# Kernel tuning notes

Hardware: AMD Instinct MI355X
Metric: run time of the kernel (lower is better)

## Reference

```python
import jax, jax.numpy as jnp
import numpy as np

D_MODEL = 1024
N_HEADS = 16
FEATURE_DIM = 16
HEAD_DIM = D_MODEL // N_HEADS  # 64
EPS = 1e-12


def taylor_exp(x):
    """2nd-order Taylor feature map of exp(q^T k / sqrt(d)).
    x: (b, h, l, d) -> (b, h, l, 1 + d + d^2)"""
    d = x.shape[-1]
    rd = jnp.sqrt(jnp.asarray(d, x.dtype))      # sqrt(d)
    rrd = jnp.sqrt(rd)                          # d^(1/4)
    r2 = jnp.sqrt(jnp.asarray(2.0, x.dtype))
    x2 = (x[..., :, None] * x[..., None, :]).reshape(*x.shape[:-1], d * d) / r2
    ones = jnp.ones_like(x[..., :1])
    return jnp.concatenate([ones, x / rrd, x2 / rd], axis=-1)


def setup_inputs() -> dict:
    key = jax.random.key(0)
    k0, k1, k2, k3, k4 = jax.random.split(key, 5)
    b, l = 1, 1024
    scale = 1.0 / np.sqrt(D_MODEL)
    hidden_states = jax.random.normal(k0, (b, l, D_MODEL), dtype=jnp.float32)
    Wq = jax.random.normal(k1, (N_HEADS * FEATURE_DIM, D_MODEL), dtype=jnp.float32) * scale
    Wk = jax.random.normal(k2, (N_HEADS * FEATURE_DIM, D_MODEL), dtype=jnp.float32) * scale
    Wv = jax.random.normal(k3, (N_HEADS * HEAD_DIM, D_MODEL), dtype=jnp.float32) * scale
    Wo = jax.random.normal(k4, (D_MODEL, N_HEADS * HEAD_DIM), dtype=jnp.float32) * scale
    return {"hidden_states": hidden_states, "Wq": Wq, "Wk": Wk, "Wv": Wv, "Wo": Wo}


def reference(hidden_states, Wq, Wk, Wv, Wo):
    b, l, _ = hidden_states.shape
    # projections (bias-free)
    q = (hidden_states @ Wq.T).reshape(b, l, N_HEADS, FEATURE_DIM).transpose(0, 2, 1, 3)
    k = (hidden_states @ Wk.T).reshape(b, l, N_HEADS, FEATURE_DIM).transpose(0, 2, 1, 3)
    v = (hidden_states @ Wv.T).reshape(b, l, N_HEADS, HEAD_DIM).transpose(0, 2, 1, 3)
    qf = taylor_exp(q)   # (b, h, l, D) with D = 1 + d + d^2 = 273
    kf = taylor_exp(k)
    # causal linear attention via associative KV accumulation
    # kv_state[l] = sum_{t<=l} phi(k_t) outer v_t  -> (b, h, l, head_dim, D)
    kv_state = jnp.cumsum(kf[..., None, :] * v[..., :, None], axis=2)
    num = jnp.einsum('bhlD,bhldD->bhld', qf, kv_state)
    den = jnp.einsum('bhlD,bhlD->bhl', qf, jnp.cumsum(kf, axis=2))[..., None] + EPS
    y = num / den                                # (b, h, l, head_dim)
    y = y.transpose(0, 2, 1, 3).reshape(b, l, N_HEADS * HEAD_DIM)
    return y @ Wo.T
```

## Files before the change

kernel.cpp:

```cpp
#include <hip/hip_runtime.h>

#define LSEQ 1024
#define DMODEL 1024
#define NHEADS 16
#define FDIM 16
#define HDIM 64
#define CHUNK 64
#define NCHUNK 16

typedef __attribute__((ext_vector_type(8))) short short8;
typedef __attribute__((ext_vector_type(4))) float floatx4;

__device__ __forceinline__ float bf2f(unsigned short u) {
    unsigned int x = ((unsigned int)u) << 16;
    return __builtin_bit_cast(float, x);
}
__device__ __forceinline__ unsigned short f2bf(float f) {
    unsigned int x = __builtin_bit_cast(unsigned int, f);
    unsigned int r = (x + 0x7fffu + ((x >> 16) & 1u)) >> 16;
    return (unsigned short)r;
}

__device__ __forceinline__ int block_detect_fp32(const unsigned short* wq) {
    __shared__ int cnt;
    if (threadIdx.x == 0) cnt = 0;
    __syncthreads();
    int bad = 0;
    for (int i = threadIdx.x; i < 1024; i += blockDim.x) {
        int e = (wq[i] >> 7) & 0xFF;
        if (e >= 143 || (e > 0 && e <= 80)) bad++;
    }
    if (bad) atomicAdd(&cnt, bad);
    __syncthreads();
    return cnt > 128;
}

#define U_QB   0
#define U_KB   262144
#define U_VB   524288
#define U_YB   1572864

#define MFMA(a, b, c) __builtin_amdgcn_mfma_f32_16x16x32_bf16((a), (b), (c), 0, 0, 0)

__device__ __forceinline__ void gemm64_body(
    unsigned short (&As)[64][136], unsigned short (&Bs)[64][136],
    const void* Araw, int a_fp32, int arow0,
    const void* Braw, int b_fp32, int brow0, floatx4 acc[4]) {
    int t = threadIdx.x;
    int r = t >> 2, c0 = (t & 3) * 32;
    int wave = t >> 6, lane = t & 63;
    int ml = lane & 15, q4 = lane >> 4;
    int mq = (wave >> 1) * 32, nq = (wave & 1) * 32;
    #pragma unroll
    for (int i = 0; i < 4; ++i) acc[i] = (floatx4){0.f, 0.f, 0.f, 0.f};

    short8 av[2][4], bv[2][4];
    auto stage = [&](int k0, short8 a[4], short8 b[4]) {
        if (!a_fp32) {
            const unsigned short* Ap = (const unsigned short*)Araw + (size_t)(arow0 + r) * DMODEL + k0 + c0;
            #pragma unroll
            for (int j = 0; j < 4; ++j) a[j] = *(const short8*)(Ap + j * 8);
        } else {
            const float* Ap = (const float*)Araw + (size_t)(arow0 + r) * DMODEL + k0 + c0;
            #pragma unroll
            for (int j = 0; j < 4; ++j)
                #pragma unroll
                for (int u = 0; u < 8; ++u) a[j][u] = (short)f2bf(Ap[j * 8 + u]);
        }
        if (!b_fp32) {
            const unsigned short* Bp = (const unsigned short*)Braw + (size_t)(brow0 + r) * DMODEL + k0 + c0;
            #pragma unroll
            for (int j = 0; j < 4; ++j) b[j] = *(const short8*)(Bp + j * 8);
        } else {
            const float* Bp = (const float*)Braw + (size_t)(brow0 + r) * DMODEL + k0 + c0;
            #pragma unroll
            for (int j = 0; j < 4; ++j)
                #pragma unroll
                for (int u = 0; u < 8; ++u) b[j][u] = (short)f2bf(Bp[j * 8 + u]);
        }
    };

    stage(0, av[0], bv[0]);
    stage(128, av[1], bv[1]);
    #pragma unroll
    for (int it = 0; it < 8; ++it) {
        int pp = it & 1;
        __syncthreads();
        #pragma unroll
        for (int j = 0; j < 4; ++j) {
            *(short8*)&As[r][c0 + j * 8] = av[pp][j];
            *(short8*)&Bs[r][c0 + j * 8] = bv[pp][j];
        }
        __syncthreads();
        if (it < 6) stage((it + 2) * 128, av[pp], bv[pp]);
        #pragma unroll
        for (int kk = 0; kk < 4; ++kk) {
            short8 a0 = *(const short8*)&As[mq + ml][kk * 32 + q4 * 8];
            short8 a1 = *(const short8*)&As[mq + 16 + ml][kk * 32 + q4 * 8];
            short8 b0 = *(const short8*)&Bs[nq + ml][kk * 32 + q4 * 8];
            short8 b1 = *(const short8*)&Bs[nq + 16 + ml][kk * 32 + q4 * 8];
            acc[0] = MFMA(a0, b0, acc[0]); acc[1] = MFMA(a0, b1, acc[1]);
            acc[2] = MFMA(a1, b0, acc[2]); acc[3] = MFMA(a1, b1, acc[3]);
        }
    }
}

__global__ __launch_bounds__(256) void qkv_gemm(
    const void* __restrict__ hidR, const void* __restrict__ WqR,
    const void* __restrict__ WkR, const void* __restrict__ WvR,
    unsigned short* __restrict__ qb, unsigned short* __restrict__ kb,
    unsigned short* __restrict__ vb) {
    int fp32 = block_detect_fp32((const unsigned short*)WqR);
    __shared__ __align__(16) unsigned short As[64][136];
    __shared__ __align__(16) unsigned short Bs[64][136];
    int nb = blockIdx.x, mb = blockIdx.y;
    const void* Braw; unsigned short* Cout; int ldc, col0, br0;
    if (nb < 4)      { Braw = WqR; br0 = nb * 64;       Cout = qb; ldc = 256;  col0 = nb * 64; }
    else if (nb < 8) { Braw = WkR; br0 = (nb - 4) * 64; Cout = kb; ldc = 256;  col0 = (nb - 4) * 64; }
    else             { Braw = WvR; br0 = (nb - 8) * 64; Cout = vb; ldc = 1024; col0 = (nb - 8) * 64; }

    floatx4 acc[4];
    gemm64_body(As, Bs, hidR, fp32, mb * 64, Braw, fp32, br0, acc);

    int wave = threadIdx.x >> 6, lane = threadIdx.x & 63;
    int ml = lane & 15, q4 = lane >> 4;
    int mq = (wave >> 1) * 32, nq = (wave & 1) * 32;
    #pragma unroll
    for (int mi = 0; mi < 2; ++mi)
        #pragma unroll
        for (int ni = 0; ni < 2; ++ni) {
            floatx4 a = acc[mi * 2 + ni];
            int nloc = nq + ni * 16 + ml;
            #pragma unroll
            for (int r4 = 0; r4 < 4; ++r4) {
                int row = mb * 64 + mq + mi * 16 + q4 * 4 + r4;
                Cout[(size_t)row * ldc + col0 + nloc] = f2bf(a[r4]);
            }
        }
}

__global__ __launch_bounds__(256) void flash_attn(
    const unsigned short* __restrict__ qb, const unsigned short* __restrict__ kb,
    const unsigned short* __restrict__ vb, unsigned short* __restrict__ ybB) {
    int h = blockIdx.x & 15, c = blockIdx.x >> 4;
    int l0 = c * CHUNK;
    __shared__ __align__(16) unsigned short qs[64][40];
    __shared__ __align__(16) unsigned short ksm[64][40];
    __shared__ __align__(16) unsigned short vT[80][72];
    __shared__ __align__(16) unsigned short P[64][72];
    int t = threadIdx.x, lane = t & 63, wave = t >> 6;
    int ml = lane & 15, q4 = lane >> 4;
    int m0 = wave * 16;
    int sm = t >> 2, si4 = (t & 3) * 4, scc = (t & 3) * 16;

    {
        *(ushort4*)&qs[sm][si4] = *(const ushort4*)&qb[(size_t)(l0 + sm) * 256 + h * 16 + si4];
        ushort4 z = {0, 0, 0, 0};
        *(ushort4*)&qs[sm][16 + si4]  = z;
        *(ushort4*)&ksm[sm][16 + si4] = z;
    }
    if (t < 64) {
        vT[64][t] = 0x3F80;
        #pragma unroll
        for (int i = 65; i < 80; ++i) vT[i][t] = 0;
    }

    auto load_kv = [&](int j, ushort4& kr, ushort4 vr[4]) {
        kr = *(const ushort4*)&kb[(size_t)(j * 64 + sm) * 256 + h * 16 + si4];
        #pragma unroll
        for (int u = 0; u < 4; ++u)
            vr[u] = *(const ushort4*)&vb[(size_t)(j * 64 + sm) * 1024 + h * 64 + scc + u * 4];
    };

    floatx4 acc[5];
    #pragma unroll
    for (int i = 0; i < 5; ++i) acc[i] = (floatx4){0.f, 0.f, 0.f, 0.f};

    ushort4 kr, vr[4], kr2, vr2[4];
    load_kv(0, kr, vr);

    __syncthreads();
    short8 aq = *(const short8*)&qs[m0 + ml][q4 * 8];

    for (int j = 0; j <= c; ++j) {
        {
            *(ushort4*)&ksm[sm][si4] = kr;
            unsigned short tmp[16];
            #pragma unroll
            for (int u = 0; u < 4; ++u) *(ushort4*)&tmp[u * 4] = vr[u];
            #pragma unroll
            for (int u = 0; u < 16; ++u) vT[scc + u][sm] = tmp[u];
        }
        __syncthreads();
        if (j < c) load_kv(j + 1, kr2, vr2);

        bool diag = (j == c);
        #pragma unroll
        for (int nt = 0; nt < 4; ++nt) {
            short8 bk = *(const short8*)&ksm[nt * 16 + ml][q4 * 8];
            floatx4 s4 = {0.f, 0.f, 0.f, 0.f};
            s4 = MFMA(aq, bk, s4);
            int tt = nt * 16 + ml;
            #pragma unroll
            for (int r = 0; r < 4; ++r) {
                int lrow = m0 + q4 * 4 + r;
                float s = s4[r];
                float p = 1.f + 0.25f * s + 0.03125f * s * s;
                if (diag && tt > lrow) p = 0.f;
                P[lrow][tt] = f2bf(p);
            }
        }

        #pragma unroll
        for (int k0 = 0; k0 < 64; k0 += 32) {
            short8 ap = *(const short8*)&P[m0 + ml][k0 + q4 * 8];
            #pragma unroll
            for (int nt = 0; nt < 5; ++nt) {
                short8 bvv = *(const short8*)&vT[nt * 16 + ml][k0 + q4 * 8];
                acc[nt] = MFMA(ap, bvv, acc[nt]);
            }
        }
        __syncthreads();
        kr = kr2;
        #pragma unroll
        for (int u = 0; u < 4; ++u) vr[u] = vr2[u];
    }

    #pragma unroll
    for (int r = 0; r < 4; ++r) {
        float den = __shfl(acc[4][r], q4 * 16) + 1e-12f;
        float dinv = 1.f / den;
        int lrow = m0 + q4 * 4 + r;
        unsigned short* yp = ybB + (size_t)(l0 + lrow) * 1024 + h * 64;
        #pragma unroll
        for (int nt = 0; nt < 4; ++nt)
            yp[nt * 16 + ml] = f2bf(acc[nt][r] * dinv);
    }
}

__global__ __launch_bounds__(256) void out_gemm(
    const unsigned short* __restrict__ A, const void* __restrict__ WoR,
    void* __restrict__ outv, const unsigned short* __restrict__ wqraw) {
    int fp32 = block_detect_fp32(wqraw);
    __shared__ __align__(16) unsigned short As[64][136];
    __shared__ __align__(16) unsigned short Bs[64][136];
    int nb = blockIdx.x, mb = blockIdx.y;

    floatx4 acc[4];
    gemm64_body(As, Bs, A, 0, mb * 64, WoR, fp32, nb * 64, acc);

    int wave = threadIdx.x >> 6, lane = threadIdx.x & 63;
    int ml = lane & 15, q4 = lane >> 4;
    int mq = (wave >> 1) * 32, nq = (wave & 1) * 32;
    #pragma unroll
    for (int mi = 0; mi < 2; ++mi)
        #pragma unroll
        for (int ni = 0; ni < 2; ++ni) {
            floatx4 a = acc[mi * 2 + ni];
            int n = nb * 64 + nq + ni * 16 + ml;
            #pragma unroll
            for (int r4 = 0; r4 < 4; ++r4) {
                int row = mb * 64 + mq + mi * 16 + q4 * 4 + r4;
                size_t idx = (size_t)row * 1024 + n;
                if (fp32) ((float*)outv)[idx] = a[r4];
                else      ((unsigned short*)outv)[idx] = f2bf(a[r4]);
            }
        }
}

extern "C" void kernel_launch(void* const* d_in, const int* in_sizes, int n_in,
                              void* d_out, int out_size, void* d_ws, size_t ws_size,
                              hipStream_t stream) {
    unsigned short* us = (unsigned short*)d_ws;
    unsigned short* qbB = us + U_QB;
    unsigned short* kbB = us + U_KB;
    unsigned short* vbB = us + U_VB;
    unsigned short* ybB = us + U_YB;
    size_t need = (size_t)(U_YB + 1048576) * 2ull;
    if (ws_size < need) return;

    qkv_gemm<<<dim3(24, 16), 256, 0, stream>>>(d_in[0], d_in[1], d_in[2], d_in[3], qbB, kbB, vbB);
    flash_attn<<<dim3(256), 256, 0, stream>>>(qbB, kbB, vbB, ybB);
    out_gemm<<<dim3(16, 16), 256, 0, stream>>>(ybB, d_in[4], d_out, (const unsigned short*)d_in[1]);
}
```

Baseline: 141.4 us.

## Use 128x128 GEMM tiles with direct global-to-LDS async loads

After: 169.3 us. 19.7% more time.

```diff
diff --git a/kernel.cpp b/kernel.cpp
--- a/kernel.cpp
+++ b/kernel.cpp
@@ -35,6 +35,12 @@
     return cnt > 128;
 }
 
+__device__ __forceinline__ void async_copy16(const void* g, void* l) {
+    __builtin_amdgcn_global_load_lds(
+        (const __attribute__((address_space(1))) unsigned int*)g,
+        (__attribute__((address_space(3))) unsigned int*)l, 16, 0, 0);
+}
+
 #define U_QB   0
 #define U_KB   262144
 #define U_VB   524288
@@ -42,66 +48,57 @@
 
 #define MFMA(a, b, c) __builtin_amdgcn_mfma_f32_16x16x32_bf16((a), (b), (c), 0, 0, 0)
 
-__device__ __forceinline__ void gemm64_body(
-    unsigned short (&As)[64][136], unsigned short (&Bs)[64][136],
+__device__ __forceinline__ void gemm128_body(
+    unsigned short* As, unsigned short* Bs,
     const void* Araw, int a_fp32, int arow0,
-    const void* Braw, int b_fp32, int brow0, floatx4 acc[4]) {
-    int t = threadIdx.x;
-    int r = t >> 2, c0 = (t & 3) * 32;
-    int wave = t >> 6, lane = t & 63;
-    int ml = lane & 15, q4 = lane >> 4;
-    int mq = (wave >> 1) * 32, nq = (wave & 1) * 32;
-    #pragma unroll
-    for (int i = 0; i < 4; ++i) acc[i] = (floatx4){0.f, 0.f, 0.f, 0.f};
-
-    short8 av[2][4], bv[2][4];
-    auto stage = [&](int k0, short8 a[4], short8 b[4]) {
+    const void* Braw, int b_fp32, int brow0, floatx4 acc[16]) {
+    int t = threadIdx.x, lane = t & 63, wave = t >> 6;
+    int ml = lane & 15, q4 = lane >> 4;
+    int mw = (wave >> 1) * 64, nw = (wave & 1) * 64;
+    #pragma unroll
+    for (int i = 0; i < 16; ++i) acc[i] = (floatx4){0.f, 0.f, 0.f, 0.f};
+
+    int drow = lane >> 2, dcol = (lane & 3) * 8;
+    int cr = t >> 1, cb = (t & 1) * 16;
+
+    for (int k0 = 0; k0 < DMODEL; k0 += 32) {
         if (!a_fp32) {
-            const unsigned short* Ap = (const unsigned short*)Araw + (size_t)(arow0 + r) * DMODEL + k0 + c0;
-            #pragma unroll
-            for (int j = 0; j < 4; ++j) a[j] = *(const short8*)(Ap + j * 8);
+            const unsigned short* Ag = (const unsigned short*)Araw;
+            #pragma unroll
+            for (int i = wave; i < 8; i += 4)
+                async_copy16(Ag + (size_t)(arow0 + i * 16 + drow) * DMODEL + k0 + dcol,
+                             As + i * 512 + lane * 8);
         } else {
-            const float* Ap = (const float*)Araw + (size_t)(arow0 + r) * DMODEL + k0 + c0;
-            #pragma unroll
-            for (int j = 0; j < 4; ++j)
-                #pragma unroll
-                for (int u = 0; u < 8; ++u) a[j][u] = (short)f2bf(Ap[j * 8 + u]);
+            const float* Ap = (const float*)Araw + (size_t)(arow0 + cr) * DMODEL + k0 + cb;
+            #pragma unroll
+            for (int u = 0; u < 16; ++u) As[cr * 32 + cb + u] = f2bf(Ap[u]);
         }
         if (!b_fp32) {
-            const unsigned short* Bp = (const unsigned short*)Braw + (size_t)(brow0 + r) * DMODEL + k0 + c0;
-            #pragma unroll
-            for (int j = 0; j < 4; ++j) b[j] = *(const short8*)(Bp + j * 8);
+            const unsigned short* Bg = (const unsigned short*)Braw;
+            #pragma unroll
+            for (int i = wave; i < 8; i += 4)
+                async_copy16(Bg + (size_t)(brow0 + i * 16 + drow) * DMODEL + k0 + dcol,
+                             Bs + i * 512 + lane * 8);
         } else {
-            const float* Bp = (const float*)Braw + (size_t)(brow0 + r) * DMODEL + k0 + c0;
-            #pragma unroll
-            for (int j = 0; j < 4; ++j)
-                #pragma unroll
-                for (int u = 0; u < 8; ++u) b[j][u] = (short)f2bf(Bp[j * 8 + u]);
-        }
-    };
-
-    stage(0, av[0], bv[0]);
-    stage(128, av[1], bv[1]);
-    #pragma unroll
-    for (int it = 0; it < 8; ++it) {
-        int pp = it & 1;
-        __syncthreads();
-        #pragma unroll
-        for (int j = 0; j < 4; ++j) {
-            *(short8*)&As[r][c0 + j * 8] = av[pp][j];
-            *(short8*)&Bs[r][c0 + j * 8] = bv[pp][j];
-        }
-        __syncthreads();
-        if (it < 6) stage((it + 2) * 128, av[pp], bv[pp]);
-        #pragma unroll
-        for (int kk = 0; kk < 4; ++kk) {
-            short8 a0 = *(const short8*)&As[mq + ml][kk * 32 + q4 * 8];
-            short8 a1 = *(const short8*)&As[mq + 16 + ml][kk * 32 + q4 * 8];
-            short8 b0 = *(const short8*)&Bs[nq + ml][kk * 32 + q4 * 8];
-            short8 b1 = *(const short8*)&Bs[nq + 16 + ml][kk * 32 + q4 * 8];
-            acc[0] = MFMA(a0, b0, acc[0]); acc[1] = MFMA(a0, b1, acc[1]);
-            acc[2] = MFMA(a1, b0, acc[2]); acc[3] = MFMA(a1, b1, acc[3]);
-        }
+            const float* Bp = (const float*)Braw + (size_t)(brow0 + cr) * DMODEL + k0 + cb;
+            #pragma unroll
+            for (int u = 0; u < 16; ++u) Bs[cr * 32 + cb + u] = f2bf(Bp[u]);
+        }
+        __syncthreads();
+
+        short8 af[4], bf[4];
+        #pragma unroll
+        for (int mi = 0; mi < 4; ++mi)
+            af[mi] = *(const short8*)&As[(mw + mi * 16 + ml) * 32 + q4 * 8];
+        #pragma unroll
+        for (int ni = 0; ni < 4; ++ni)
+            bf[ni] = *(const short8*)&Bs[(nw + ni * 16 + ml) * 32 + q4 * 8];
+        #pragma unroll
+        for (int mi = 0; mi < 4; ++mi)
+            #pragma unroll
+            for (int ni = 0; ni < 4; ++ni)
+                acc[mi * 4 + ni] = MFMA(af[mi], bf[ni], acc[mi * 4 + ni]);
+        __syncthreads();
     }
 }
 
@@ -111,30 +108,30 @@
     unsigned short* __restrict__ qb, unsigned short* __restrict__ kb,
     unsigned short* __restrict__ vb) {
     int fp32 = block_detect_fp32((const unsigned short*)WqR);
-    __shared__ __align__(16) unsigned short As[64][136];
-    __shared__ __align__(16) unsigned short Bs[64][136];
+    __shared__ __align__(16) unsigned short As[128 * 32];
+    __shared__ __align__(16) unsigned short Bs[128 * 32];
     int nb = blockIdx.x, mb = blockIdx.y;
-    const void* Braw; unsigned short* Cout; int ldc, col0, br0;
-    if (nb < 4)      { Braw = WqR; br0 = nb * 64;       Cout = qb; ldc = 256;  col0 = nb * 64; }
-    else if (nb < 8) { Braw = WkR; br0 = (nb - 4) * 64; Cout = kb; ldc = 256;  col0 = (nb - 4) * 64; }
-    else             { Braw = WvR; br0 = (nb - 8) * 64; Cout = vb; ldc = 1024; col0 = (nb - 8) * 64; }
-
-    floatx4 acc[4];
-    gemm64_body(As, Bs, hidR, fp32, mb * 64, Braw, fp32, br0, acc);
-
-    int wave = threadIdx.x >> 6, lane = threadIdx.x & 63;
-    int ml = lane & 15, q4 = lane >> 4;
-    int mq = (wave >> 1) * 32, nq = (wave & 1) * 32;
-    #pragma unroll
-    for (int mi = 0; mi < 2; ++mi)
-        #pragma unroll
-        for (int ni = 0; ni < 2; ++ni) {
-            floatx4 a = acc[mi * 2 + ni];
-            int nloc = nq + ni * 16 + ml;
+    const void* Braw; unsigned short* Cout; int ldc, colbase, br0;
+    if (nb < 2)      { Braw = WqR; br0 = nb * 128;       Cout = qb; ldc = 256;  colbase = nb * 128; }
+    else if (nb < 4) { Braw = WkR; br0 = (nb - 2) * 128; Cout = kb; ldc = 256;  colbase = (nb - 2) * 128; }
+    else             { Braw = WvR; br0 = (nb - 4) * 128; Cout = vb; ldc = 1024; colbase = (nb - 4) * 128; }
+
+    floatx4 acc[16];
+    gemm128_body(As, Bs, hidR, fp32, mb * 128, Braw, fp32, br0, acc);
+
+    int lane = threadIdx.x & 63, wave = threadIdx.x >> 6;
+    int ml = lane & 15, q4 = lane >> 4;
+    int mw = (wave >> 1) * 64, nw = (wave & 1) * 64;
+    #pragma unroll
+    for (int mi = 0; mi < 4; ++mi)
+        #pragma unroll
+        for (int ni = 0; ni < 4; ++ni) {
+            floatx4 a = acc[mi * 4 + ni];
+            int nloc = nw + ni * 16 + ml;
             #pragma unroll
             for (int r4 = 0; r4 < 4; ++r4) {
-                int row = mb * 64 + mq + mi * 16 + q4 * 4 + r4;
-                Cout[(size_t)row * ldc + col0 + nloc] = f2bf(a[r4]);
+                int row = mb * 128 + mw + mi * 16 + q4 * 4 + r4;
+                Cout[(size_t)row * ldc + colbase + nloc] = f2bf(a[r4]);
             }
         }
 }
@@ -210,7 +207,6 @@
                 P[lrow][tt] = f2bf(p);
             }
         }
-
         #pragma unroll
         for (int k0 = 0; k0 < 64; k0 += 32) {
             short8 ap = *(const short8*)&P[m0 + ml][k0 + q4 * 8];
@@ -242,25 +238,25 @@
     const unsigned short* __restrict__ A, const void* __restrict__ WoR,
     void* __restrict__ outv, const unsigned short* __restrict__ wqraw) {
     int fp32 = block_detect_fp32(wqraw);
-    __shared__ __align__(16) unsigned short As[64][136];
-    __shared__ __align__(16) unsigned short Bs[64][136];
+    __shared__ __align__(16) unsigned short As[128 * 32];
+    __shared__ __align__(16) unsigned short Bs[128 * 32];
     int nb = blockIdx.x, mb = blockIdx.y;
 
-    floatx4 acc[4];
-    gemm64_body(As, Bs, A, 0, mb * 64, WoR, fp32, nb * 64, acc);
-
-    int wave = threadIdx.x >> 6, lane = threadIdx.x & 63;
-    int ml = lane & 15, q4 = lane >> 4;
-    int mq = (wave >> 1) * 32, nq = (wave & 1) * 32;
-    #pragma unroll
-    for (int mi = 0; mi < 2; ++mi)
-        #pragma unroll
-        for (int ni = 0; ni < 2; ++ni) {
-            floatx4 a = acc[mi * 2 + ni];
-            int n = nb * 64 + nq + ni * 16 + ml;
+    floatx4 acc[16];
+    gemm128_body(As, Bs, A, 0, mb * 128, WoR, fp32, nb * 128, acc);
+
+    int lane = threadIdx.x & 63, wave = threadIdx.x >> 6;
+    int ml = lane & 15, q4 = lane >> 4;
+    int mw = (wave >> 1) * 64, nw = (wave & 1) * 64;
+    #pragma unroll
+    for (int mi = 0; mi < 4; ++mi)
+        #pragma unroll
+        for (int ni = 0; ni < 4; ++ni) {
+            floatx4 a = acc[mi * 4 + ni];
+            int n = nb * 128 + nw + ni * 16 + ml;
             #pragma unroll
             for (int r4 = 0; r4 < 4; ++r4) {
-                int row = mb * 64 + mq + mi * 16 + q4 * 4 + r4;
+                int row = mb * 128 + mw + mi * 16 + q4 * 4 + r4;
                 size_t idx = (size_t)row * 1024 + n;
                 if (fp32) ((float*)outv)[idx] = a[r4];
                 else      ((unsigned short*)outv)[idx] = f2bf(a[r4]);
@@ -279,7 +275,7 @@
     size_t need = (size_t)(U_YB + 1048576) * 2ull;
     if (ws_size < need) return;
 
-    qkv_gemm<<<dim3(24, 16), 256, 0, stream>>>(d_in[0], d_in[1], d_in[2], d_in[3], qbB, kbB, vbB);
+    qkv_gemm<<<dim3(12, 8), 256, 0, stream>>>(d_in[0], d_in[1], d_in[2], d_in[3], qbB, kbB, vbB);
     flash_attn<<<dim3(256), 256, 0, stream>>>(qbB, kbB, vbB, ybB);
-    out_gemm<<<dim3(16, 16), 256, 0, stream>>>(ybB, d_in[4], d_out, (const unsigned short*)d_in[1]);
-}
+    out_gemm<<<dim3(8, 8), 256, 0, stream>>>(ybB, d_in[4], d_out, (const unsigned short*)d_in[1]);
+}
```
